# Kernel tuning notes

Measured on AMD Instinct MI355X. Metric: run time of the kernel, lower is better.

## Reference

```python
import jax, jax.numpy as jnp
from jax import lax
import numpy as np

V, EMB, ELMO, WORD, H, B, R, L = 11322, 300, 1024, 512, 512, 32, 10, 20


def setup_inputs():
    key = jax.random.key(0)
    ks = jax.random.split(key, 24)

    def n(k, shape, s=0.02):
        return jax.random.normal(k, shape, dtype=jnp.float32) * s

    inp = {}
    inp["ques"] = jax.random.randint(ks[0], (B, R, L), 0, V)
    inp["hist"] = jax.random.randint(ks[1], (B, R, 2 * L), 0, V)
    inp["ques_len"] = jax.random.randint(ks[2], (B, R), 1, L + 1)
    inp["hist_len"] = jax.random.randint(ks[3], (B, R), 1, 2 * L + 1)
    inp["img_feat"] = n(ks[4], (B, 36, 2048), 1.0)
    inp["v_relations"] = n(ks[5], (B, 36, 36, 512), 1.0)
    inp["w_emb"] = n(ks[6], (V, EMB))          # GloVe/numberbatch table
    inp["elmo_emb"] = n(ks[7], (V, ELMO))      # frozen ELMo table
    inp["Wc"] = n(ks[8], (WORD, ELMO))         # embed_change Linear
    inp["bc"] = jnp.zeros((WORD,), jnp.float32)
    IN0 = EMB + WORD                            # LSTM layer-0 input size = 812
    names = ["q_Wih0", "q_Whh0", "q_b0", "q_Wih1", "q_Whh1", "q_b1",
             "h_Wih0", "h_Whh0", "h_b0", "h_Wih1", "h_Whh1", "h_b1"]
    shapes = [(4 * H, IN0), (4 * H, H), (4 * H,), (4 * H, H), (4 * H, H), (4 * H,)] * 2
    for i, (nm, sh) in enumerate(zip(names, shapes)):
        inp[nm] = n(ks[9 + i], sh, 0.04)
    return inp


def lstm_layer(x, Wih, Whh, b):
    # x: [N, T, In] -> all hidden states [N, T, H]; PyTorch gate order i,f,g,o
    N = x.shape[0]
    Hh = Whh.shape[1]
    xproj = jnp.einsum('nti,gi->ntg', x, Wih) + b  # [N, T, 4H]

    def step(carry, xp):
        h, c = carry
        gates = xp + h @ Whh.T
        i, f, g, o = jnp.split(gates, 4, axis=-1)
        c = jax.nn.sigmoid(f) * c + jax.nn.sigmoid(i) * jnp.tanh(g)
        h = jax.nn.sigmoid(o) * jnp.tanh(c)
        return (h, c), h

    h0 = jnp.zeros((N, Hh), x.dtype)
    _, hs = lax.scan(step, (h0, h0), jnp.swapaxes(xproj, 0, 1))
    return jnp.swapaxes(hs, 0, 1)


def encode(tokens, lens, w_emb, elmo_emb, Wc, bc, Wih0, Whh0, b0, Wih1, Whh1, b1):
    # Embedding lookup + elmo->word projection, 2-layer LSTM, take h at t = len-1
    Ntok = tokens.shape[0]
    emb = w_emb[tokens]                         # [N, T, 300]
    elmo = elmo_emb[tokens] @ Wc.T + bc         # [N, T, 512] (dropout off: eval)
    x = jnp.concatenate([emb, elmo], axis=-1)   # [N, T, 812]
    h1 = lstm_layer(x, Wih0, Whh0, b0)
    h2 = lstm_layer(h1, Wih1, Whh1, b1)
    return h2[jnp.arange(Ntok), lens - 1]       # DynamicRNN: last valid hidden


def reference(ques, hist, ques_len, hist_len, img_feat, v_relations, w_emb, elmo_emb, Wc, bc,
              q_Wih0, q_Whh0, q_b0, q_Wih1, q_Whh1, q_b1,
              h_Wih0, h_Whh0, h_b0, h_Wih1, h_Whh1, h_b1):
    Bq, Rr, Ll = ques.shape
    ques_embed = encode(ques.reshape(Bq * Rr, Ll), ques_len.reshape(-1),
                        w_emb, elmo_emb, Wc, bc,
                        q_Wih0, q_Whh0, q_b0, q_Wih1, q_Whh1, q_b1).reshape(Bq, Rr, -1)
    hist_embed = encode(hist.reshape(Bq * Rr, 2 * Ll), hist_len.reshape(-1),
                        w_emb, elmo_emb, Wc, bc,
                        h_Wih0, h_Whh0, h_b0, h_Wih1, h_Whh1, h_b1).reshape(Bq, Rr, -1)
    # Vectorized form of the Python double loop + pad_sequence:
    # f_history[b, i, j] = hist_embed[b, j] if j <= i else 0   -> [B, R, R, H]
    tri = jnp.tril(jnp.ones((Rr, Rr), hist_embed.dtype))
    f_history = hist_embed[:, None, :, :] * tri[None, :, :, None]
    # masks exactly as t_rel.abs().sum(-1).bool() on the broadcast tensors
    m = (jnp.abs(f_history).sum(-1) != 0)       # [B, R, R]
    # t_rel[b,i,j,k,:] = f_history[b,i,j,:] zeroed where tmp (=f_history[b,i,k]) is zero
    t_rel = f_history[:, :, :, None, :] * m[:, :, None, :, None]
    tmp = f_history[:, :, None, :, :] * m[:, :, :, None, None]
    text_rel = jnp.concatenate([t_rel, tmp], axis=-1)  # [B, R, R, R, 2H]
    return ques_embed, text_rel
```

## Files before the change

kernel.cpp:

```cpp
#include <hip/hip_runtime.h>
#include <math.h>

#define NSEQ 320
#define HDIM 512
#define G4   2048
#define EMBD 300
#define ELMOD 1024
#define XPAD 832
#define BUFU (160*1024)

typedef __attribute__((ext_vector_type(8))) short bf16x8;
typedef __attribute__((ext_vector_type(4))) float f32x4;
typedef __attribute__((ext_vector_type(4))) unsigned int u32x4;
typedef __attribute__((ext_vector_type(2))) unsigned int u32x2;
typedef unsigned short ushort_t;

__device__ __forceinline__ float sigmoidf_(float x) { return 1.0f / (1.0f + expf(-x)); }

__device__ __forceinline__ ushort_t f2bf(float f) {
    unsigned u = __float_as_uint(f);
    u = (u + 0x7FFFu + ((u >> 16) & 1u)) >> 16;
    return (ushort_t)u;
}
__device__ __forceinline__ unsigned pack2(float a, float b) {
    return (unsigned)f2bf(a) | ((unsigned)f2bf(b) << 16);
}

struct ConvPack {
    const float* src[9];
    ushort_t* dst[9];
    int srcCols[9], dstStride[9], dstOff[9], fillCols[9];
    long base[10];
};

__global__ __launch_bounds__(256) void conv_all_kernel(ConvPack P)
{
    long gid = (long)blockIdx.x * 256 + threadIdx.x;
    if (gid >= P.base[9]) return;
    int job = 0;
    #pragma unroll
    for (int j = 1; j < 9; ++j) if (gid >= P.base[j]) job = j;
    int e  = (int)(gid - P.base[job]);
    int fc = P.fillCols[job];
    int r  = e / fc;
    int ci = e - r * fc;
    int sc = P.srcCols[job];
    float v = (ci < sc) ? P.src[job][(size_t)r * sc + ci] : 0.0f;
    P.dst[job][(size_t)r * P.dstStride[job] + P.dstOff[job] + ci] = f2bf(v);
}

__global__ __launch_bounds__(128) void emb_gather_kernel(
    const int* __restrict__ ques, const int* __restrict__ hist,
    const float* __restrict__ w_emb, ushort_t* __restrict__ Xb)
{
    int n = blockIdx.x;
    int tokid = (n < 6400) ? ques[n] : hist[n - 6400];
    int t = threadIdx.x;
    ushort_t* dst = Xb + (size_t)n * XPAD;
    if (t < 75) {
        const float4* src = (const float4*)(w_emb + (size_t)tokid * EMBD);
        float4 v = src[t];
        dst[4*t+0] = f2bf(v.x); dst[4*t+1] = f2bf(v.y);
        dst[4*t+2] = f2bf(v.z); dst[4*t+3] = f2bf(v.w);
    } else if (t >= 108) {
        dst[812 + (t - 108)] = 0;
    }
}

__global__ __launch_bounds__(256) void gemm_ff_kernel(
    const ushort_t* __restrict__ Ab, const float* __restrict__ Af,
    const int* __restrict__ tok, int strideA,
    const ushort_t* __restrict__ W, const float* __restrict__ bias,
    ushort_t* __restrict__ C, int strideC, int K, int remap)
{
    __shared__ ushort_t As[64 * 40];
    __shared__ ushort_t Bs[64 * 40];
    const int m0 = blockIdx.y * 64;
    const int n0 = blockIdx.x * 64;
    const int tid = threadIdx.x;
    const int r  = tid >> 2;
    const int kq = (tid & 3) << 3;

    const ushort_t* arow_b = nullptr;
    const float*    arow_f = nullptr;
    if (Af) arow_f = Af + (size_t)tok[m0 + r] * strideA + kq;
    else    arow_b = Ab + (size_t)(m0 + r) * strideA + kq;
    const ushort_t* brow = W + (size_t)(n0 + r) * K + kq;

    const int lane = tid & 63;
    const int w = tid >> 6;
    const int wm = w & 1, wn = w >> 1;
    const int kc = (lane >> 4) << 3;

    f32x4 acc[2][2];
    #pragma unroll
    for (int f = 0; f < 2; ++f)
        #pragma unroll
        for (int g = 0; g < 2; ++g)
            acc[f][g] = (f32x4){0.f, 0.f, 0.f, 0.f};

    for (int k0 = 0; k0 < K; k0 += 32) {
        if (Af) {
            float4 v0 = ((const float4*)(arow_f + k0))[0];
            float4 v1 = ((const float4*)(arow_f + k0))[1];
            uint4 p; p.x = pack2(v0.x, v0.y); p.y = pack2(v0.z, v0.w);
            p.z = pack2(v1.x, v1.y); p.w = pack2(v1.z, v1.w);
            *(uint4*)&As[r*40 + kq] = p;
        } else {
            *(uint4*)&As[r*40 + kq] = *(const uint4*)(arow_b + k0);
        }
        *(uint4*)&Bs[r*40 + kq] = *(const uint4*)(brow + k0);
        __syncthreads();
        bf16x8 af[2], bfr[2];
        #pragma unroll
        for (int f = 0; f < 2; ++f)
            af[f] = *(const bf16x8*)&As[(wm*32 + f*16 + (lane & 15))*40 + kc];
        #pragma unroll
        for (int g = 0; g < 2; ++g)
            bfr[g] = *(const bf16x8*)&Bs[(wn*32 + g*16 + (lane & 15))*40 + kc];
        #pragma unroll
        for (int f = 0; f < 2; ++f)
            #pragma unroll
            for (int g = 0; g < 2; ++g)
                acc[f][g] = __builtin_amdgcn_mfma_f32_16x16x32_bf16(af[f], bfr[g], acc[f][g], 0, 0, 0);
        __syncthreads();
    }

    #pragma unroll
    for (int f = 0; f < 2; ++f) {
        #pragma unroll
        for (int g = 0; g < 2; ++g) {
            int col = n0 + wn*32 + g*16 + (lane & 15);
            float bv = bias[col];
            int colw = remap ? ((col & 511) * 4 + (col >> 9)) : col;
            #pragma unroll
            for (int i = 0; i < 4; ++i) {
                int row = m0 + wm*32 + f*16 + ((lane >> 4) << 2) + i;
                C[(size_t)row * strideC + colw] = f2bf(acc[f][g][i] + bv);
            }
        }
    }
}

__global__ __launch_bounds__(256) void gemm_xp_kernel(
    const ushort_t* __restrict__ A,
    const ushort_t* __restrict__ W,
    const float* __restrict__ bias,
    ushort_t* __restrict__ C)
{
    __shared__ ushort_t As[128 * 32];
    __shared__ ushort_t Bs[128 * 32];
    const int m0 = blockIdx.y * 128;
    const int n0 = blockIdx.x * 128;
    const int tid = threadIdx.x;
    const int w = tid >> 6, lane = tid & 63;
    const int wm = w & 1, wn = w >> 1;
    const int cc = lane & 15, kg = lane >> 4;
    const int srow = lane >> 2;
    const int skc  = lane & 3;

    f32x4 acc[4][4];
    #pragma unroll
    for (int f = 0; f < 4; ++f)
        #pragma unroll
        for (int g = 0; g < 4; ++g)
            acc[f][g] = (f32x4){0.f, 0.f, 0.f, 0.f};

    for (int k0 = 0; k0 < XPAD; k0 += 32) {
        __syncthreads();
        #pragma unroll
        for (int i = 0; i < 2; ++i) {
            const int r = w*16 + i*64;
            const ushort_t* ga = A + (size_t)(m0 + r + srow) * XPAD + k0 + skc*8;
            ushort_t* la = &As[r * 32];
            __builtin_amdgcn_global_load_lds(
                (const __attribute__((address_space(1))) unsigned int*)ga,
                (__attribute__((address_space(3))) unsigned int*)la, 16, 0, 0);
            const ushort_t* gb = W + (size_t)(n0 + r + srow) * XPAD + k0 + skc*8;
            ushort_t* lb = &Bs[r * 32];
            __builtin_amdgcn_global_load_lds(
                (const __attribute__((address_space(1))) unsigned int*)gb,
                (__attribute__((address_space(3))) unsigned int*)lb, 16, 0, 0);
        }
        asm volatile("s_waitcnt vmcnt(0)");
        __syncthreads();
        bf16x8 af[4], bfr[4];
        #pragma unroll
        for (int f = 0; f < 4; ++f)
            af[f] = *(const bf16x8*)&As[(wm*64 + f*16 + cc)*32 + kg*8];
        #pragma unroll
        for (int g = 0; g < 4; ++g)
            bfr[g] = *(const bf16x8*)&Bs[(wn*64 + g*16 + cc)*32 + kg*8];
        #pragma unroll
        for (int f = 0; f < 4; ++f)
            #pragma unroll
            for (int g = 0; g < 4; ++g)
                acc[f][g] = __builtin_amdgcn_mfma_f32_16x16x32_bf16(af[f], bfr[g], acc[f][g], 0, 0, 0);
    }

    #pragma unroll
    for (int f = 0; f < 4; ++f) {
        #pragma unroll
        for (int g = 0; g < 4; ++g) {
            int col = n0 + wn*64 + g*16 + cc;
            float bv = bias[col];
            int colw = (col & 511) * 4 + (col >> 9);
            #pragma unroll
            for (int i = 0; i < 4; ++i) {
                int row = m0 + wm*64 + f*16 + kg*4 + i;
                C[(size_t)row * G4 + colw] = f2bf(acc[f][g][i] + bv);
            }
        }
    }
}

struct PCellN {
    ushort_t* rot;
    const ushort_t* B;
    const ushort_t* xp;
    const float* bias;
    float* hlast;
    const int* lens;
    int* flags;
    int* pflag;
    int K, T, layer;
};
struct PPackN { PCellN cell[8]; };

template<int N> __device__ __forceinline__ void vmwait() {
    if constexpr      (N == 0)  asm volatile("s_waitcnt vmcnt(0)"  ::: "memory");
    else if constexpr (N == 1)  asm volatile("s_waitcnt vmcnt(1)"  ::: "memory");
    else if constexpr (N == 2)  asm volatile("s_waitcnt vmcnt(2)"  ::: "memory");
    else if constexpr (N == 3)  asm volatile("s_waitcnt vmcnt(3)"  ::: "memory");
    else if constexpr (N == 4)  asm volatile("s_waitcnt vmcnt(4)"  ::: "memory");
    else if constexpr (N == 5)  asm volatile("s_waitcnt vmcnt(5)"  ::: "memory");
    else if constexpr (N == 6)  asm volatile("s_waitcnt vmcnt(6)"  ::: "memory");
    else if constexpr (N == 7)  asm volatile("s_waitcnt vmcnt(7)"  ::: "memory");
    else if constexpr (N == 8)  asm volatile("s_waitcnt vmcnt(8)"  ::: "memory");
    else if constexpr (N == 9)  asm volatile("s_waitcnt vmcnt(9)"  ::: "memory");
    else if constexpr (N == 10) asm volatile("s_waitcnt vmcnt(10)" ::: "memory");
    else if constexpr (N == 11) asm volatile("s_waitcnt vmcnt(11)" ::: "memory");
    else if constexpr (N == 12) asm volatile("s_waitcnt vmcnt(12)" ::: "memory");
    else if constexpr (N == 13) asm volatile("s_waitcnt vmcnt(13)" ::: "memory");
    else if constexpr (N == 14) asm volatile("s_waitcnt vmcnt(14)" ::: "memory");
    else                        asm volatile("s_waitcnt vmcnt(15)" ::: "memory");
}

template<int C, int NQ, int D>
__device__ __forceinline__ void aissN(uint4 (&ap)[D][NQ],
    const ushort_t* baseX, const ushort_t* baseH, const int* aoff)
{
    const ushort_t* b_ = (C * 32 < 512) ? baseX : baseH;
    #pragma unroll
    for (int q = 0; q < NQ; ++q)
        asm volatile("global_load_dwordx4 %0, %1, off"
            : "=v"(ap[C % D][q])
            : "v"((const char*)b_ + aoff[q] + C * 64));
}

template<int C, int D, int NQ>
__device__ __forceinline__ void prologueN(uint4 (&ap)[D][NQ],
    const ushort_t* bX, const ushort_t* bH, const int* aoff)
{
    if constexpr (C < D) {
        aissN<C, NQ, D>(ap, bX, bH, aoff);
        prologueN<C + 1, D, NQ>(ap, bX, bH, aoff);
    }
}

template<int C, int NC, int NQ, int D>
__device__ __forceinline__ void chunksN(uint4 (&ap)[D][NQ], f32x4 (&acc)[NQ][4],
    const ushort_t* bX, const ushort_t* bH, const int* aoff,
    const ushort_t* Bs, int cc, int kg, int swz)
{
    if constexpr (C < NC) {
        constexpr int infl = (NC - 1 - C) > (D - 1) ? (D - 1) : (NC - 1 - C);
        vmwait<infl * NQ>();
        __builtin_amdgcn_sched_barrier(0);
        bf16x8 bfr[4];
        #pragma unroll
        for (int g = 0; g < 4; ++g) {
            int boff = ((g*16 + cc) * (NC*64) + C*64 + kg*16) ^ swz;
            bfr[g] = *(const bf16x8*)((const char*)Bs + boff);
        }
        #pragma unroll
        for (int q = 0; q < NQ; ++q)
            #pragma unroll
            for (int g = 0; g < 4; ++g)
                acc[q][g] = __builtin_amdgcn_mfma_f32_16x16x32_bf16(
                    *(const bf16x8*)&ap[C % D][q], bfr[g], acc[q][g], 0, 0, 0);
        if constexpr (C + D < NC) aissN<C + D, NQ, D>(ap, bX, bH, aoff);
        chunksN<C + 1, NC, NQ, D>(ap, acc, bX, bH, aoff, Bs, cc, kg, swz);
    }
}

template<int NC, int NQ, int D>
__device__ __forceinline__ void step_work(
    const ushort_t* __restrict__ baseX,
    const ushort_t* __restrict__ baseH,
    const ushort_t* __restrict__ Bs,
    const ushort_t* __restrict__ xp,
    const float* __restrict__ bias_r,
    ushort_t* __restrict__ Ost,
    float* __restrict__ hlast,
    const unsigned* __restrict__ lr,
    float (&creg)[3][4],
    int t, int T, int tq0, int lane, int j)
{
    const int cc = lane & 15, kg = lane >> 4;
    const int swz = (cc & 7) << 4;

    int aoff[NQ];
    #pragma unroll
    for (int q = 0; q < NQ; ++q)
        aoff[q] = ((tq0 + q)*16 + cc)*2048 + kg*16;

    u32x2 xpk[NQ][4];
    if (xp) {
        #pragma unroll
        for (int q = 0; q < NQ; ++q)
            #pragma unroll
            for (int i = 0; i < 4; ++i) {
                const int n = (tq0 + q)*16 + kg*4 + i;
                asm volatile("global_load_dwordx2 %0, %1, off"
                    : "=v"(xpk[q][i])
                    : "v"((const char*)xp + ((size_t)n*T + t)*4096 + (size_t)j*8));
            }
    }

    f32x4 acc[NQ][4];
    #pragma unroll
    for (int q = 0; q < NQ; ++q)
        #pragma unroll
        for (int g = 0; g < 4; ++g)
            acc[q][g] = (f32x4){0.f, 0.f, 0.f, 0.f};

    uint4 ap[D][NQ];
    prologueN<0, D, NQ>(ap, baseX, baseH, aoff);
    chunksN<0, NC, NQ, D>(ap, acc, baseX, baseH, aoff, Bs, cc, kg, swz);
    __builtin_amdgcn_sched_barrier(0);

    #pragma unroll
    for (int q = 0; q < NQ; ++q) {
        const unsigned lq = lr[q];
        #pragma unroll
        for (int i = 0; i < 4; ++i) {
            const int n = (tq0 + q)*16 + kg*4 + i;
            float g0 = acc[q][0][i], g1 = acc[q][1][i];
            float g2 = acc[q][2][i], g3 = acc[q][3][i];
            if (xp) {
                u32x2 xv = xpk[q][i];
                g0 += __uint_as_float(xv.x << 16);
                g1 += __uint_as_float(xv.x & 0xFFFF0000u);
                g2 += __uint_as_float(xv.y << 16);
                g3 += __uint_as_float(xv.y & 0xFFFF0000u);
            } else {
                g0 += bias_r[0]; g1 += bias_r[1];
                g2 += bias_r[2]; g3 += bias_r[3];
            }
            float cn = sigmoidf_(g1) * creg[q][i] + sigmoidf_(g0) * tanhf(g2);
            creg[q][i] = cn;
            float h = sigmoidf_(g3) * tanhf(cn);
            unsigned hb = (unsigned)f2bf(h);
            unsigned pb = (unsigned)__shfl_xor((int)hb, 1);
            if ((cc & 1) == 0) {
                ushort_t* oa = Ost + (size_t)n * 1024 + j;
                asm volatile("global_store_dword %0, %1, off sc0 sc1"
                             :: "v"(oa), "v"(hb | (pb << 16)));
            }
            if (hlast && t == (int)((lq >> (8*i)) & 0xFF) - 1)
                hlast[(size_t)n * HDIM + j] = h;
        }
    }
}

__global__ __launch_bounds__(256) void lstm_persist_kernel(PPackN P)
{
    const int inst = blockIdx.x & 7;
    const int blk  = blockIdx.x >> 3;
    const PCellN cl = P.cell[inst];

    const int tid  = threadIdx.x;
    const int w    = tid >> 6;
    const int lane = tid & 63;
    const int cc   = lane & 15;
    const int kg   = lane >> 4;
    const int j0   = blk * 16;
    const int j    = j0 + cc;
    const int K = cl.K, T = cl.T;
    const int nq  = (w < 2) ? 3 : 2;
    const int tq0 = (w < 2) ? w*3 : 6 + (w - 2)*2;

    __shared__ ushort_t Bs[64 * 1024];

    {
        const int CH = K >> 3;
        const int tot = 64 * CH;
        for (int idx = tid; idx < tot; idx += 256) {
            int r = idx / CH, ch = idx - r * CH;
            int gr = (r >> 4) * HDIM + j0 + (r & 15);
            int dst = (idx * 16) ^ ((r & 7) << 4);
            *(u32x4*)((char*)Bs + dst) = *(const u32x4*)(cl.B + (size_t)gr * K + ch * 8);
        }
    }

    float bias_r[4] = {0.f, 0.f, 0.f, 0.f};
    if (cl.bias) {
        #pragma unroll
        for (int g = 0; g < 4; ++g) bias_r[g] = cl.bias[g * HDIM + j];
    }

    unsigned lr[3] = {0u, 0u, 0u};
    #pragma unroll
    for (int q = 0; q < 3; ++q) {
        if (q < nq) {
            unsigned pkd = 0;
            #pragma unroll
            for (int i = 0; i < 4; ++i)
                pkd |= ((unsigned)cl.lens[(tq0 + q)*16 + kg*4 + i] & 0xFF) << (8*i);
            lr[q] = pkd;
        }
    }

    float creg[3][4];
    #pragma unroll
    for (int q = 0; q < 3; ++q)
        #pragma unroll
        for (int i = 0; i < 4; ++i) creg[q][i] = 0.f;

    __syncthreads();

    for (int ss = 0; ss <= T; ++ss) {
        const bool active = cl.layer ? (ss >= 1) : (ss < T);
        if (active) {
            const int t = cl.layer ? (ss - 1) : ss;
            const ushort_t* baseX; const ushort_t* baseH; ushort_t* Ost;
            if (cl.layer == 0) {
                baseX = cl.rot + (size_t)t * BUFU;
                baseH = baseX;
                Ost   = cl.rot + (size_t)(t + 1) * BUFU;
            } else {
                baseX = cl.rot + (size_t)(t + 1) * BUFU;
                baseH = cl.rot + (size_t)t * BUFU;
                Ost   = cl.rot + (size_t)(t + 1) * BUFU + HDIM;
            }
            if (K == 512) {
                if (w < 2) step_work<16,3,6>(baseX, baseH, Bs, cl.xp, bias_r, Ost, cl.hlast, lr, creg, t, T, tq0, lane, j);
                else       step_work<16,2,8>(baseX, baseH, Bs, cl.xp, bias_r, Ost, cl.hlast, lr, creg, t, T, tq0, lane, j);
            } else {
                if (w < 2) step_work<32,3,6>(baseX, baseH, Bs, cl.xp, bias_r, Ost, cl.hlast, lr, creg, t, T, tq0, lane, j);
                else       step_work<32,2,8>(baseX, baseH, Bs, cl.xp, bias_r, Ost, cl.hlast, lr, creg, t, T, tq0, lane, j);
            }
        }
        if (ss < T) {
            asm volatile("s_waitcnt vmcnt(0)" ::: "memory");
            __syncthreads();
            if (tid == 0) {
                int* fa = cl.flags + blk;
                int vv = ss + 1;
                asm volatile("global_store_dword %0, %1, off sc0 sc1"
                             :: "v"(fa), "v"(vv) : "memory");
            }
            if (w == 0) {
                const int* fa = cl.flags + (lane & 31);
                int spins = 0; bool ok;
                do {
                    int v;
                    asm volatile("global_load_dword %0, %1, off sc0 sc1"
                                 : "=v"(v) : "v"(fa) : "memory");
                    asm volatile("s_waitcnt vmcnt(0)" ::: "memory");
                    ok = (bool)__all(v >= ss + 1);
                    if (!ok) __builtin_amdgcn_s_sleep(1);
                } while (!ok && ++spins < (1 << 20));
                if (cl.layer == 0) {
                    if (blk == 0 && lane == 0) {
                        int vv = ss + 1;
                        asm volatile("global_store_dword %0, %1, off sc0 sc1"
                                     :: "v"(cl.pflag), "v"(vv) : "memory");
                    }
                } else if (lane == 0) {
                    int spins2 = 0; int pv;
                    do {
                        asm volatile("global_load_dword %0, %1, off sc0 sc1"
                                     : "=v"(pv) : "v"((const int*)cl.pflag) : "memory");
                        asm volatile("s_waitcnt vmcnt(0)" ::: "memory");
                        if (pv < ss + 1) __builtin_amdgcn_s_sleep(1);
                    } while (pv < ss + 1 && ++spins2 < (1 << 20));
                }
            }
            __syncthreads();
        }
    }
}

__global__ __launch_bounds__(64) void nz_kernel(
    const float* __restrict__ he, int* __restrict__ nz)
{
    int rr = blockIdx.x;
    int lane = threadIdx.x;
    const float* row = he + (size_t)rr * HDIM;
    bool any = false;
    for (int k = lane; k < HDIM; k += 64) any |= (row[k] != 0.0f);
    unsigned long long b = __ballot(any);
    if (lane == 0) nz[rr] = (b != 0ull) ? 1 : 0;
}

__global__ __launch_bounds__(256) void expand_kernel(
    const float* __restrict__ he, const int* __restrict__ nz,
    float* __restrict__ out)
{
    int blk = blockIdx.x;
    int k = blk % 10;
    int j = (blk / 10) % 10;
    int i = (blk / 100) % 10;
    int b = blk / 1000;
    int tid = threadIdx.x;
    float4* o = (float4*)(out + (size_t)blk * 1024);
    float4 z; z.x = z.y = z.z = z.w = 0.0f;
    if (tid < 128) {
        bool m = (j <= i) && (k <= i) && (nz[b*10 + k] != 0);
        float4 v = m ? ((const float4*)(he + (size_t)(b*10 + j) * HDIM))[tid] : z;
        o[tid] = v;
    } else {
        int c = tid - 128;
        bool m = (k <= i) && (j <= i) && (nz[b*10 + j] != 0);
        float4 v = m ? ((const float4*)(he + (size_t)(b*10 + k) * HDIM))[c] : z;
        o[128 + c] = v;
    }
}

extern "C" void kernel_launch(void* const* d_in, const int* in_sizes, int n_in,
                              void* d_out, int out_size, void* d_ws, size_t ws_size,
                              hipStream_t stream)
{
    (void)in_sizes; (void)n_in; (void)out_size; (void)ws_size;
    const int* ques     = (const int*)d_in[0];
    const int* hist     = (const int*)d_in[1];
    const int* ques_len = (const int*)d_in[2];
    const int* hist_len = (const int*)d_in[3];
    const float* w_emb  = (const float*)d_in[6];
    const float* elmo   = (const float*)d_in[7];
    const float* Wc     = (const float*)d_in[8];
    const float* bc     = (const float*)d_in[9];

    char* ws = (char*)d_ws;
    size_t off = 0;
    auto alloc = [&](size_t bytes) { char* p = ws + off; off += (bytes + 255) & ~(size_t)255; return p; };
    ushort_t* XP0bf = (ushort_t*)alloc((size_t)19200 * G4 * 2);

    const size_t rotSlice = (size_t)41 * BUFU * 2;
    char* uni = alloc(4 * rotSlice);
    ushort_t* Xb = (ushort_t*)uni;
    auto rotPtr = [&](int s, int v) { return (ushort_t*)(uni + (size_t)(s*2 + v) * rotSlice); };

    ushort_t* Wcb = (ushort_t*)alloc((size_t)HDIM * ELMOD * 2);
    ushort_t *Wih0b[2], *Whh0b[2], *Wcat[2];
    for (int s = 0; s < 2; ++s) {
        Wih0b[s] = (ushort_t*)alloc((size_t)G4 * XPAD * 2);
        Whh0b[s] = (ushort_t*)alloc((size_t)G4 * HDIM * 2);
        Wcat[s]  = (ushort_t*)alloc((size_t)G4 * ELMOD * 2);
    }
    int* ctrs = (int*)alloc(4096);
    float* he = (float*)alloc((size_t)NSEQ * HDIM * 4);
    int* nzb  = (int*)alloc(NSEQ * 4);

    float* out = (float*)d_out;
    float* ques_embed = out;
    float* text_rel   = out + (size_t)NSEQ * HDIM;

    const int rowoff[2] = {0, 6400};
    const int TT[2] = {20, 40};
    const int* lensp[2] = {ques_len, hist_len};

    ConvPack CP;
    {
        int ji = 0; long base = 0;
        auto addJob = [&](const float* src, ushort_t* dst, int sc, int ds, int doff, int fc, int rows) {
            CP.src[ji] = src; CP.dst[ji] = dst; CP.srcCols[ji] = sc; CP.dstStride[ji] = ds;
            CP.dstOff[ji] = doff; CP.fillCols[ji] = fc; CP.base[ji] = base;
            base += (long)fc * rows; ++ji;
        };
        addJob(Wc, Wcb, ELMOD, ELMOD, 0, ELMOD, HDIM);
        for (int s = 0; s < 2; ++s) {
            addJob((const float*)d_in[10 + 6*s], Wih0b[s], 812,  XPAD,  0,    XPAD, G4);
            addJob((const float*)d_in[11 + 6*s], Whh0b[s], HDIM, HDIM,  0,    HDIM, G4);
            addJob((const float*)d_in[13 + 6*s], Wcat[s],  HDIM, ELMOD, 0,    HDIM, G4);
            addJob((const float*)d_in[14 + 6*s], Wcat[s],  HDIM, ELMOD, HDIM, HDIM, G4);
        }
        CP.base[9] = base;
        int nblk = (int)((base + 255) / 256);
        conv_all_kernel<<<nblk, 256, 0, stream>>>(CP);
    }

    emb_gather_kernel<<<19200, 128, 0, stream>>>(ques, hist, w_emb, Xb);
    for (int s = 0; s < 2; ++s) {
        int Ntok = NSEQ * TT[s];
        ushort_t* XbS = Xb + (size_t)rowoff[s] * XPAD;
        const int* tok = s ? hist : ques;
        gemm_ff_kernel<<<dim3(HDIM/64, Ntok/64), 256, 0, stream>>>(
            nullptr, elmo, tok, ELMOD, Wcb, bc, XbS + EMBD, XPAD, ELMOD, 0);
        const float* b0 = (const float*)d_in[12 + 6*s];
        gemm_xp_kernel<<<dim3(G4/128, Ntok/128), 256, 0, stream>>>(
            XbS, Wih0b[s], b0, XP0bf + (size_t)rowoff[s] * G4);
    }

    hipMemsetAsync(ctrs, 0, 4096, stream);
    for (int s = 0; s < 2; ++s)
        for (int v = 0; v < 2; ++v)
            hipMemsetAsync(rotPtr(s, v), 0, (size_t)BUFU * 2, stream);

    PPackN P;
    for (int layer = 0; layer < 2; ++layer)
        for (int s = 0; s < 2; ++s)
            for (int v = 0; v < 2; ++v) {
                int inst = layer*4 + s*2 + v;
                PCellN& c = P.cell[inst];
                c.rot   = rotPtr(s, v);
                c.B     = layer ? Wcat[s] : Whh0b[s];
                c.xp    = layer ? nullptr
                                : XP0bf + (size_t)(rowoff[s] + v*160*TT[s]) * G4;
                c.bias  = layer ? (const float*)d_in[15 + 6*s] : nullptr;
                c.hlast = layer ? ((s ? he : ques_embed) + (size_t)v*160*HDIM) : nullptr;
                c.lens  = lensp[s] + v*160;
                c.flags = ctrs + inst * 32;
                c.pflag = ctrs + 512 + (s*2 + v) * 32;
                c.K = layer ? ELMOD : HDIM;
                c.T = TT[s];
                c.layer = layer;
            }
    lstm_persist_kernel<<<256, 256, 0, stream>>>(P);

    nz_kernel<<<NSEQ, 64, 0, stream>>>(he, nzb);
    expand_kernel<<<32000, 256, 0, stream>>>(he, nzb, text_rel);
}
```

Measured before the change: 975.1 us.

## Prefetch LSTM input projections into LDS, merge spin waits, fuse ELMo GEMMs

The persistent LSTM kernel now prefetches the next timestep's precomputed input projection into LDS with global_load_lds, right after the current step's work, so the load overlaps the barrier wait instead of sitting on the critical path. The layer-1 wait on the layer-0 progress flag is folded into the same wavefront-wide spin poll over the peer flags, which removes a second serial spin loop. The two per-stream ELMo projection GEMMs are merged into one launch over a concatenated token array written by the gather kernel. In exchange, the kernel uses more LDS and the prefetch adds a memory wait before the barrier.

Measured after the change: 1.106 ms. 1.13x slower.

```diff
diff --git a/kernel.cpp b/kernel.cpp
--- a/kernel.cpp
+++ b/kernel.cpp
@@ -12,7 +12,6 @@
 typedef __attribute__((ext_vector_type(8))) short bf16x8;
 typedef __attribute__((ext_vector_type(4))) float f32x4;
 typedef __attribute__((ext_vector_type(4))) unsigned int u32x4;
-typedef __attribute__((ext_vector_type(2))) unsigned int u32x2;
 typedef unsigned short ushort_t;
 
 __device__ __forceinline__ float sigmoidf_(float x) { return 1.0f / (1.0f + expf(-x)); }
@@ -51,7 +50,8 @@
 
 __global__ __launch_bounds__(128) void emb_gather_kernel(
     const int* __restrict__ ques, const int* __restrict__ hist,
-    const float* __restrict__ w_emb, ushort_t* __restrict__ Xb)
+    const float* __restrict__ w_emb, ushort_t* __restrict__ Xb,
+    int* __restrict__ tokcat)
 {
     int n = blockIdx.x;
     int tokid = (n < 6400) ? ques[n] : hist[n - 6400];
@@ -64,6 +64,7 @@
         dst[4*t+2] = f2bf(v.z); dst[4*t+3] = f2bf(v.w);
     } else if (t >= 108) {
         dst[812 + (t - 108)] = 0;
+        if (t == 108) tokcat[n] = tokid;
     }
 }
 
@@ -294,18 +295,39 @@
     }
 }
 
+__device__ __forceinline__ void prefetch_xp(
+    const ushort_t* xp, unsigned* xps, int T, int tq0, int nq,
+    int kg, int j, int wv, int t)
+{
+    for (int q = 0; q < nq; ++q) {
+        #pragma unroll
+        for (int i = 0; i < 4; ++i) {
+            const int n = (tq0 + q)*16 + kg*4 + i;
+            const char* src = (const char*)xp + ((size_t)n*T + t)*4096 + (size_t)j*8;
+            #pragma unroll
+            for (int w2 = 0; w2 < 2; ++w2) {
+                unsigned* dst = xps + ((q*4 + i)*2 + w2)*256 + wv*64;
+                __builtin_amdgcn_global_load_lds(
+                    (const __attribute__((address_space(1))) unsigned int*)(src + w2*4),
+                    (__attribute__((address_space(3))) unsigned int*)dst, 4, 0, 0);
+            }
+        }
+    }
+}
+
 template<int NC, int NQ, int D>
 __device__ __forceinline__ void step_work(
     const ushort_t* __restrict__ baseX,
     const ushort_t* __restrict__ baseH,
     const ushort_t* __restrict__ Bs,
-    const ushort_t* __restrict__ xp,
+    const unsigned* __restrict__ xpsT,
+    int hasXp,
     const float* __restrict__ bias_r,
     ushort_t* __restrict__ Ost,
     float* __restrict__ hlast,
     const unsigned* __restrict__ lr,
     float (&creg)[3][4],
-    int t, int T, int tq0, int lane, int j)
+    int t, int tq0, int lane, int j)
 {
     const int cc = lane & 15, kg = lane >> 4;
     const int swz = (cc & 7) << 4;
@@ -314,19 +336,6 @@
     #pragma unroll
     for (int q = 0; q < NQ; ++q)
         aoff[q] = ((tq0 + q)*16 + cc)*2048 + kg*16;
-
-    u32x2 xpk[NQ][4];
-    if (xp) {
-        #pragma unroll
-        for (int q = 0; q < NQ; ++q)
-            #pragma unroll
-            for (int i = 0; i < 4; ++i) {
-                const int n = (tq0 + q)*16 + kg*4 + i;
-                asm volatile("global_load_dwordx2 %0, %1, off"
-                    : "=v"(xpk[q][i])
-                    : "v"((const char*)xp + ((size_t)n*T + t)*4096 + (size_t)j*8));
-            }
-    }
 
     f32x4 acc[NQ][4];
     #pragma unroll
@@ -348,12 +357,13 @@
             const int n = (tq0 + q)*16 + kg*4 + i;
             float g0 = acc[q][0][i], g1 = acc[q][1][i];
             float g2 = acc[q][2][i], g3 = acc[q][3][i];
-            if (xp) {
-                u32x2 xv = xpk[q][i];
-                g0 += __uint_as_float(xv.x << 16);
-                g1 += __uint_as_float(xv.x & 0xFFFF0000u);
-                g2 += __uint_as_float(xv.y << 16);
-                g3 += __uint_as_float(xv.y & 0xFFFF0000u);
+            if (hasXp) {
+                unsigned lo = xpsT[((q*4 + i)*2 + 0)*256];
+                unsigned hi = xpsT[((q*4 + i)*2 + 1)*256];
+                g0 += __uint_as_float(lo << 16);
+                g1 += __uint_as_float(lo & 0xFFFF0000u);
+                g2 += __uint_as_float(hi << 16);
+                g3 += __uint_as_float(hi & 0xFFFF0000u);
             } else {
                 g0 += bias_r[0]; g1 += bias_r[1];
                 g2 += bias_r[2]; g3 += bias_r[3];
@@ -392,6 +402,8 @@
     const int tq0 = (w < 2) ? w*3 : 6 + (w - 2)*2;
 
     __shared__ ushort_t Bs[64 * 1024];
+    __shared__ unsigned xps[24 * 256];
+    const unsigned* xpsT = xps + tid;
 
     {
         const int CH = K >> 3;
@@ -404,6 +416,9 @@
         }
     }
 
+    const int hasXp = (cl.xp != nullptr);
+    if (hasXp) prefetch_xp(cl.xp, xps, T, tq0, nq, kg, j, w, 0);
+
     float bias_r[4] = {0.f, 0.f, 0.f, 0.f};
     if (cl.bias) {
         #pragma unroll
@@ -428,6 +443,7 @@
         #pragma unroll
         for (int i = 0; i < 4; ++i) creg[q][i] = 0.f;
 
+    asm volatile("s_waitcnt vmcnt(0)" ::: "memory");
     __syncthreads();
 
     for (int ss = 0; ss <= T; ++ss) {
@@ -445,12 +461,14 @@
                 Ost   = cl.rot + (size_t)(t + 1) * BUFU + HDIM;
             }
             if (K == 512) {
-                if (w < 2) step_work<16,3,6>(baseX, baseH, Bs, cl.xp, bias_r, Ost, cl.hlast, lr, creg, t, T, tq0, lane, j);
-                else       step_work<16,2,8>(baseX, baseH, Bs, cl.xp, bias_r, Ost, cl.hlast, lr, creg, t, T, tq0, lane, j);
+                if (w < 2) step_work<16,3,6>(baseX, baseH, Bs, xpsT, hasXp, bias_r, Ost, cl.hlast, lr, creg, t, tq0, lane, j);
+                else       step_work<16,2,8>(baseX, baseH, Bs, xpsT, hasXp, bias_r, Ost, cl.hlast, lr, creg, t, tq0, lane, j);
             } else {
-                if (w < 2) step_work<32,3,6>(baseX, baseH, Bs, cl.xp, bias_r, Ost, cl.hlast, lr, creg, t, T, tq0, lane, j);
-                else       step_work<32,2,8>(baseX, baseH, Bs, cl.xp, bias_r, Ost, cl.hlast, lr, creg, t, T, tq0, lane, j);
-            }
+                if (w < 2) step_work<32,3,6>(baseX, baseH, Bs, xpsT, hasXp, bias_r, Ost, cl.hlast, lr, creg, t, tq0, lane, j);
+                else       step_work<32,2,8>(baseX, baseH, Bs, xpsT, hasXp, bias_r, Ost, cl.hlast, lr, creg, t, tq0, lane, j);
+            }
+            if (hasXp && t + 1 < T)
+                prefetch_xp(cl.xp, xps, T, tq0, nq, kg, j, w, t + 1);
         }
         if (ss < T) {
             asm volatile("s_waitcnt vmcnt(0)" ::: "memory");
@@ -462,30 +480,21 @@
                              :: "v"(fa), "v"(vv) : "memory");
             }
             if (w == 0) {
-                const int* fa = cl.flags + (lane & 31);
+                const int* pa = (lane < 32) ? (cl.flags + lane) : cl.pflag;
+                const bool chk = (lane < 32) || (cl.layer == 1 && lane == 32);
                 int spins = 0; bool ok;
                 do {
                     int v;
                     asm volatile("global_load_dword %0, %1, off sc0 sc1"
-                                 : "=v"(v) : "v"(fa) : "memory");
+                                 : "=v"(v) : "v"(pa) : "memory");
                     asm volatile("s_waitcnt vmcnt(0)" ::: "memory");
-                    ok = (bool)__all(v >= ss + 1);
+                    ok = (bool)__all(!chk || v >= ss + 1);
                     if (!ok) __builtin_amdgcn_s_sleep(1);
                 } while (!ok && ++spins < (1 << 20));
-                if (cl.layer == 0) {
-                    if (blk == 0 && lane == 0) {
-                        int vv = ss + 1;
-                        asm volatile("global_store_dword %0, %1, off sc0 sc1"
-                                     :: "v"(cl.pflag), "v"(vv) : "memory");
-                    }
-                } else if (lane == 0) {
-                    int spins2 = 0; int pv;
-                    do {
-                        asm volatile("global_load_dword %0, %1, off sc0 sc1"
-                                     : "=v"(pv) : "v"((const int*)cl.pflag) : "memory");
-                        asm volatile("s_waitcnt vmcnt(0)" ::: "memory");
-                        if (pv < ss + 1) __builtin_amdgcn_s_sleep(1);
-                    } while (pv < ss + 1 && ++spins2 < (1 << 20));
+                if (cl.layer == 0 && blk == 0 && lane == 0) {
+                    int vv = ss + 1;
+                    asm volatile("global_store_dword %0, %1, off sc0 sc1"
+                                 :: "v"(cl.pflag), "v"(vv) : "memory");
                 }
             }
             __syncthreads();
@@ -560,6 +569,7 @@
         Whh0b[s] = (ushort_t*)alloc((size_t)G4 * HDIM * 2);
         Wcat[s]  = (ushort_t*)alloc((size_t)G4 * ELMOD * 2);
     }
+    int* tokcat = (int*)alloc(19200 * 4);
     int* ctrs = (int*)alloc(4096);
     float* he = (float*)alloc((size_t)NSEQ * HDIM * 4);
     int* nzb  = (int*)alloc(NSEQ * 4);
@@ -592,13 +602,12 @@
         conv_all_kernel<<<nblk, 256, 0, stream>>>(CP);
     }
 
-    emb_gather_kernel<<<19200, 128, 0, stream>>>(ques, hist, w_emb, Xb);
+    emb_gather_kernel<<<19200, 128, 0, stream>>>(ques, hist, w_emb, Xb, tokcat);
+    gemm_ff_kernel<<<dim3(HDIM/64, 19200/64), 256, 0, stream>>>(
+        nullptr, elmo, tokcat, ELMOD, Wcb, bc, Xb + EMBD, XPAD, ELMOD, 0);
     for (int s = 0; s < 2; ++s) {
         int Ntok = NSEQ * TT[s];
         ushort_t* XbS = Xb + (size_t)rowoff[s] * XPAD;
-        const int* tok = s ? hist : ques;
-        gemm_ff_kernel<<<dim3(HDIM/64, Ntok/64), 256, 0, stream>>>(
-            nullptr, elmo, tok, ELMOD, Wcb, bc, XbS + EMBD, XPAD, ELMOD, 0);
         const float* b0 = (const float*)d_in[12 + 6*s];
         gemm_xp_kernel<<<dim3(G4/128, Ntok/128), 256, 0, stream>>>(
             XbS, Wih0b[s], b0, XP0bf + (size_t)rowoff[s] * G4);
```
